# Performance work log

Hardware: AMD Instinct MI355X
Metric: run time of the kernel (lower is better)

Reference implementation:

```python
import jax, jax.numpy as jnp
import numpy as np
import math

IN_CH = 32
OUT_CH = 32
NODE_NUM = 24
BATCH = 32768
# skeleton edges: self-loops + chain (parent -> child), matching init_kwargs
_SRC = list(range(24)) + list(range(23))
_DST = list(range(24)) + list(range(1, 24))


def _build_mask():
    # block mask: block (dst, src) of size [OUT_CH, IN_CH] set to 1 per edge
    m = np.zeros((OUT_CH * NODE_NUM, IN_CH * NODE_NUM), dtype=np.float32)
    for s, d in zip(_SRC, _DST):
        m[OUT_CH * d:OUT_CH * (d + 1), IN_CH * s:IN_CH * (s + 1)] = 1.0
    return jnp.asarray(m)


def setup_inputs() -> dict:
    key = jax.random.key(0)
    kx, kw, kb = jax.random.split(key, 3)
    mask = _build_mask()
    dim = IN_CH * NODE_NUM
    # kaiming-uniform-like per-block init approximated by scaled normal; only
    # values inside mask blocks matter (forward multiplies by mask anyway)
    weight = jax.random.normal(kw, (OUT_CH * NODE_NUM, dim), dtype=jnp.float32) * (1.0 / math.sqrt(IN_CH))
    bound = 1.0 / math.sqrt(dim)
    bias = jax.random.uniform(kb, (OUT_CH * NODE_NUM,), dtype=jnp.float32, minval=-bound, maxval=bound)
    x = jax.random.normal(kx, (BATCH, dim), dtype=jnp.float32)
    return {"x": x, "weight": weight, "bias": bias, "mask": mask}


def reference(x, weight, bias, mask):
    # F.linear(x, weight * mask, bias) == x @ (weight*mask)^T + bias
    w = weight * mask
    return jnp.einsum("bi,oi->bo", x, w) + bias
```

## Files before the change

### kernel.cpp

```cpp
#include <hip/hip_runtime.h>
#include <hip/hip_bf16.h>


typedef __bf16 bf16x8 __attribute__((ext_vector_type(8)));
typedef float  f32x4  __attribute__((ext_vector_type(4)));

#define DIM 768
#define NFRAG (24 * 2 * 2)

__device__ __forceinline__ bf16x8 cvt8(const float* __restrict__ p) {
    float4 lo = *(const float4*)p;
    float4 hi = *(const float4*)(p + 4);
    bf16x8 r;
    r[0] = (__bf16)lo.x; r[1] = (__bf16)lo.y; r[2] = (__bf16)lo.z; r[3] = (__bf16)lo.w;
    r[4] = (__bf16)hi.x; r[5] = (__bf16)hi.y; r[6] = (__bf16)hi.z; r[7] = (__bf16)hi.w;
    return r;
}

__device__ __forceinline__ bf16x8 cvt8r(float4 lo, float4 hi) {
    bf16x8 r;
    r[0] = (__bf16)lo.x; r[1] = (__bf16)lo.y; r[2] = (__bf16)lo.z; r[3] = (__bf16)lo.w;
    r[4] = (__bf16)hi.x; r[5] = (__bf16)hi.y; r[6] = (__bf16)hi.z; r[7] = (__bf16)hi.w;
    return r;
}

__global__ void prepack_w_kernel(const float* __restrict__ w, bf16x8* __restrict__ ws)
{
    const int fid = blockIdx.x * 256 + threadIdx.x;
    const int lane = fid & 63;
    const int ni   = (fid >> 6) & 1;
    const int kt   = (fid >> 7) & 1;
    const int d    = fid >> 8;
    const int quad = lane >> 4, l16 = lane & 15;

    bf16x8 v;
    if (d == 0 && kt == 0) {
#pragma unroll
        for (int j = 0; j < 8; ++j) v[j] = (__bf16)0.f;
    } else {
        const float* src = w + (long)(32 * d + 16 * ni + l16) * DIM
                             + (32 * d - 32 + 32 * kt + 8 * quad);
        v = cvt8(src);
    }
    ws[fid] = v;
}

__global__ __launch_bounds__(512, 4)
void skeleton_linear_kernel(const float* __restrict__ x,
                            const float* __restrict__ bias,
                            const bf16x8* __restrict__ wfrag,
                            float* __restrict__ out)
{
    const int tid  = threadIdx.x;
    const int lane = tid & 63;
    const int wave = tid >> 6;
    const int quad = lane >> 4;
    const int l16  = lane & 15;
    const long row = (long)blockIdx.x * 16 + l16;

    const float* xr = x + row * DIM + 8 * quad;
    float4 lo[4], hi[4];
#pragma unroll
    for (int s = 0; s < 4; ++s) {
        int kb = 32 * (3 * wave - 1 + s);
        if (kb < 0) kb = 0;
        lo[s] = *(const float4*)(xr + kb);
        hi[s] = *(const float4*)(xr + kb + 4);
    }
    bf16x8 xf[4];
#pragma unroll
    for (int s = 0; s < 4; ++s) xf[s] = cvt8r(lo[s], hi[s]);

    float* orow = out + row * DIM;
#pragma unroll
    for (int i = 0; i < 3; ++i) {
        const int d = 3 * wave + i;
        f32x4 acc0 = *(const f32x4*)(bias + 32 * d + 4 * quad);
        f32x4 acc1 = *(const f32x4*)(bias + 32 * d + 16 + 4 * quad);
#pragma unroll
        for (int kt = 0; kt < 2; ++kt) {
            const int fb = (d * 2 + kt) * 2 * 64 + lane;
            acc0 = __builtin_amdgcn_mfma_f32_16x16x32_bf16(wfrag[fb],      xf[i + kt], acc0, 0, 0, 0);
            acc1 = __builtin_amdgcn_mfma_f32_16x16x32_bf16(wfrag[fb + 64], xf[i + kt], acc1, 0, 0, 0);
        }
        *(f32x4*)(orow + 32 * d + 4 * quad)      = acc0;
        *(f32x4*)(orow + 32 * d + 16 + 4 * quad) = acc1;
    }
}

extern "C" void kernel_launch(void* const* d_in, const int* in_sizes, int n_in,
                              void* d_out, int out_size, void* d_ws, size_t ws_size,
                              hipStream_t stream) {
    const float* x    = (const float*)d_in[0];
    const float* w    = (const float*)d_in[1];
    const float* bias = (const float*)d_in[2];
    float* out = (float*)d_out;

    bf16x8* wpack = (bf16x8*)d_ws;

    prepack_w_kernel<<<NFRAG * 64 / 256, 256, 0, stream>>>(w, wpack);

    const int BATCH = 32768;
    dim3 grid(BATCH / 16);
    skeleton_linear_kernel<<<grid, 512, 0, stream>>>(x, bias, wpack, out);
}
```

Baseline: 195.8 us.

## Make linear kernel persistent with register-prefetched next row tile

The grid shrinks from 2048 blocks to 512, and each block now processes four 16-row tiles strided across the batch. The x loads for the next tile are issued before the MFMAs and stores of the current tile, and bias is loaded once per block instead of per tile. The goal is to overlap global-load latency with compute and cut per-block launch and bias-load overhead. The costs are higher register pressure and fewer resident blocks to hide memory latency, on a kernel that is mostly memory-bound.

```diff
diff --git a/kernel.cpp b/kernel.cpp
--- a/kernel.cpp
+++ b/kernel.cpp
@@ -7,6 +7,7 @@
 
 #define DIM 768
 #define NFRAG (24 * 2 * 2)
+#define NBLK 512
 
 __device__ __forceinline__ bf16x8 cvt8(const float* __restrict__ p) {
     float4 lo = *(const float4*)p;
@@ -56,35 +57,65 @@
     const int wave = tid >> 6;
     const int quad = lane >> 4;
     const int l16  = lane & 15;
-    const long row = (long)blockIdx.x * 16 + l16;
 
-    const float* xr = x + row * DIM + 8 * quad;
+    f32x4 b0[3], b1[3];
+#pragma unroll
+    for (int i = 0; i < 3; ++i) {
+        const int d = 3 * wave + i;
+        b0[i] = *(const f32x4*)(bias + 32 * d + 4 * quad);
+        b1[i] = *(const f32x4*)(bias + 32 * d + 16 + 4 * quad);
+    }
+
+    int kb[4];
+#pragma unroll
+    for (int s = 0; s < 4; ++s) {
+        int k = 32 * (3 * wave - 1 + s);
+        kb[s] = k < 0 ? 0 : k;
+    }
+
+    const long ROWSTEP = (long)NBLK * 16;
+    const long row0 = (long)blockIdx.x * 16 + l16;
+
+    const float* xr = x + row0 * DIM + 8 * quad;
+    float*       orow = out + row0 * DIM;
+
     float4 lo[4], hi[4];
 #pragma unroll
     for (int s = 0; s < 4; ++s) {
-        int kb = 32 * (3 * wave - 1 + s);
-        if (kb < 0) kb = 0;
-        lo[s] = *(const float4*)(xr + kb);
-        hi[s] = *(const float4*)(xr + kb + 4);
+        lo[s] = *(const float4*)(xr + kb[s]);
+        hi[s] = *(const float4*)(xr + kb[s] + 4);
     }
-    bf16x8 xf[4];
+
 #pragma unroll
-    for (int s = 0; s < 4; ++s) xf[s] = cvt8r(lo[s], hi[s]);
+    for (int t = 0; t < 4; ++t) {
+        bf16x8 xf[4];
+#pragma unroll
+        for (int s = 0; s < 4; ++s) xf[s] = cvt8r(lo[s], hi[s]);
 
-    float* orow = out + row * DIM;
+        if (t < 3) {
+            const float* xn = xr + (long)(t + 1) * ROWSTEP * DIM;
 #pragma unroll
-    for (int i = 0; i < 3; ++i) {
-        const int d = 3 * wave + i;
-        f32x4 acc0 = *(const f32x4*)(bias + 32 * d + 4 * quad);
-        f32x4 acc1 = *(const f32x4*)(bias + 32 * d + 16 + 4 * quad);
+            for (int s = 0; s < 4; ++s) {
+                lo[s] = *(const float4*)(xn + kb[s]);
+                hi[s] = *(const float4*)(xn + kb[s] + 4);
+            }
+        }
+
+        float* op = orow + (long)t * ROWSTEP * DIM;
 #pragma unroll
-        for (int kt = 0; kt < 2; ++kt) {
-            const int fb = (d * 2 + kt) * 2 * 64 + lane;
-            acc0 = __builtin_amdgcn_mfma_f32_16x16x32_bf16(wfrag[fb],      xf[i + kt], acc0, 0, 0, 0);
-            acc1 = __builtin_amdgcn_mfma_f32_16x16x32_bf16(wfrag[fb + 64], xf[i + kt], acc1, 0, 0, 0);
+        for (int i = 0; i < 3; ++i) {
+            const int d = 3 * wave + i;
+            f32x4 acc0 = b0[i];
+            f32x4 acc1 = b1[i];
+#pragma unroll
+            for (int kt = 0; kt < 2; ++kt) {
+                const int fb = (d * 2 + kt) * 2 * 64 + lane;
+                acc0 = __builtin_amdgcn_mfma_f32_16x16x32_bf16(wfrag[fb],      xf[i + kt], acc0, 0, 0, 0);
+                acc1 = __builtin_amdgcn_mfma_f32_16x16x32_bf16(wfrag[fb + 64], xf[i + kt], acc1, 0, 0, 0);
+            }
+            *(f32x4*)(op + 32 * d + 4 * quad)      = acc0;
+            *(f32x4*)(op + 32 * d + 16 + 4 * quad) = acc1;
         }
-        *(f32x4*)(orow + 32 * d + 4 * quad)      = acc0;
-        *(f32x4*)(orow + 32 * d + 16 + 4 * quad) = acc1;
     }
 }
 
@@ -100,7 +131,6 @@
 
     prepack_w_kernel<<<NFRAG * 64 / 256, 256, 0, stream>>>(w, wpack);
 
-    const int BATCH = 32768;
-    dim3 grid(BATCH / 16);
+    dim3 grid(NBLK);
     skeleton_linear_kernel<<<grid, 512, 0, stream>>>(x, bias, wpack, out);
 }
```

Result: slower. 215.5 us (+10.1%).
